# Kernel tuning notes

Measured on AMD Instinct MI355X. Metric: run time of the kernel, lower is better.

The kernel has to match this reference:

```python
import math
import jax, jax.numpy as jnp
from jax import lax
import numpy as np

NUM_POINTS = 256      # K sampled points
HIDDEN_DIM = 768
NUM_FREQS = 10
INPUT_DIM = 3 * 2 * NUM_FREQS  # 60


def _fps_indices(pts, k):
    """Furthest point sampling indices for a single cloud pts: [N,3] -> [k] int32.
    Standard iterative FPS starting from index 0."""
    n = pts.shape[0]
    idxs0 = jnp.zeros((k,), dtype=jnp.int32)
    dists0 = jnp.full((n,), jnp.inf, dtype=pts.dtype)

    def body(i, state):
        idxs, dists = state
        last = pts[idxs[i - 1]]                       # [3]
        d = jnp.sum((pts - last) ** 2, axis=-1)       # [N]
        dists = jnp.minimum(dists, d)
        idxs = idxs.at[i].set(jnp.argmax(dists).astype(jnp.int32))
        return (idxs, dists)

    idxs, _ = lax.fori_loop(1, k, body, (idxs0, dists0))
    return idxs


def setup_inputs() -> dict:
    key = jax.random.key(0)
    k1, k2, k3 = jax.random.split(key, 3)
    B, N = 32, 262144
    point_cloud = jax.random.normal(k1, (B, N, 3), dtype=jnp.float32)
    # Xavier-uniform Linear weight [out, in], zero bias (matches _init_weights)
    limit = math.sqrt(6.0 / (INPUT_DIM + HIDDEN_DIM))
    W = jax.random.uniform(k2, (HIDDEN_DIM, INPUT_DIM), jnp.float32, -limit, limit)
    b = jnp.zeros((HIDDEN_DIM,), dtype=jnp.float32)
    return {"point_cloud": point_cloud, "W": W, "b": b}


def reference(point_cloud, W, b):
    B = point_cloud.shape[0]
    # sanitize non-finite (matches torch.where(isfinite, x, 0))
    pc = jnp.where(jnp.isfinite(point_cloud), point_cloud, 0.0)

    # --- furthest point sampling (indices are non-differentiable) ---
    idxs = jax.vmap(lambda p: _fps_indices(lax.stop_gradient(p), NUM_POINTS))(pc)  # [B,K]
    sampled = jnp.take_along_axis(pc, idxs[:, :, None], axis=1)  # [B,K,3]

    # --- per-sample normalization: center then scale by max bbox dim ---
    centroid = jnp.mean(sampled, axis=1, keepdims=True)           # [B,1,3]
    centered = sampled - centroid                                  # [B,K,3]
    bbox = jnp.max(centered, axis=1) - jnp.min(centered, axis=1)   # [B,3]
    max_dim = jnp.max(bbox, axis=-1)                               # [B]
    scale = jnp.where(max_dim > 1e-8, max_dim, 1.0)
    normed = centered / scale[:, None, None]                       # [B,K,3]

    # --- Fourier encoding: sin/cos of coords * 2^f * pi ---
    freqs = jnp.power(2.0, jnp.arange(NUM_FREQS, dtype=jnp.float32))  # [F]
    scaled = normed[..., None] * freqs * jnp.float32(math.pi)         # [B,K,3,F]
    enc = jnp.stack([jnp.sin(scaled), jnp.cos(scaled)], axis=-1)      # [B,K,3,F,2]
    enc = enc.reshape(B, NUM_POINTS, INPUT_DIM)                       # [B,K,60]

    # --- linear projection (torch Linear: x @ W.T + b) ---
    return jnp.einsum('bkd,hd->bkh', enc, W) + b                      # [B,K,768]
```

## Files before the change

### kernel.cpp

```cpp
#include <hip/hip_runtime.h>

#define BATCH 32
#define NPTS  262144
#define KSAMP 256
#define NF    10
#define INDIM 60
#define HID   768

#define NBLK_PER_B 8
#define SLICE (NPTS/NBLK_PER_B)
#define REG_G 4
#define LDS_G 3

#define PI_F 3.14159274101257324f
#define PAY56 0x00FFFFFFFFFFFFFFull

typedef float v2f __attribute__((ext_vector_type(2)));

__device__ float g_px[BATCH*NPTS];
__device__ float g_py[BATCH*NPTS];
__device__ float g_pz[BATCH*NPTS];
__device__ float g_samp[BATCH*KSAMP*3];
__device__ float g_enc[(size_t)BATCH*KSAMP*INDIM];
__device__ float g_Wt[INDIM*HID];
__device__ unsigned long long g_slot[BATCH][2][NBLK_PER_B];

__device__ __forceinline__ float san(float v){
  float m = v*0.0f;
  return (m == 0.0f) ? v : 0.0f;
}

__device__ __forceinline__ unsigned long long shfl64_xor(unsigned long long v, int m){
  unsigned lo = __shfl_xor((unsigned)v, m);
  unsigned hi = __shfl_xor((unsigned)(v>>32), m);
  return ((unsigned long long)hi<<32)|lo;
}
__device__ __forceinline__ unsigned long long shfl64(unsigned long long v, int src){
  unsigned lo = __shfl((unsigned)v, src);
  unsigned hi = __shfl((unsigned)(v>>32), src);
  return ((unsigned long long)hi<<32)|lo;
}

__global__ __launch_bounds__(256) void region_prepass(const float* __restrict__ pc){
  int bid = blockIdx.x;
  int b   = bid >> 5;
  int rem = bid & 31;
  int q   = rem*1024 + threadIdx.x*4;
  int s   = q >> 12;
  int o   = q & 4095;
  int p   = s*SLICE + 7*4096 + o;
  const float* src = pc + ((size_t)b*NPTS + p)*3;
  float4 A = *(const float4*)(src);
  float4 Bv= *(const float4*)(src+4);
  float4 C = *(const float4*)(src+8);
  float v[12] = {A.x,A.y,A.z,A.w,Bv.x,Bv.y,Bv.z,Bv.w,C.x,C.y,C.z,C.w};
#pragma unroll
  for (int j=0;j<12;j++) v[j] = san(v[j]);
  size_t base = (size_t)b*NPTS + p;
  *(float4*)(g_px+base) = make_float4(v[0],v[3],v[6],v[9]);
  *(float4*)(g_py+base) = make_float4(v[1],v[4],v[7],v[10]);
  *(float4*)(g_pz+base) = make_float4(v[2],v[5],v[8],v[11]);
}

__global__ __launch_bounds__(256) void wtrans(const float* __restrict__ W){
  int idx = blockIdx.x*256 + threadIdx.x;
  int d = idx / HID;
  int h = idx - d*HID;
  g_Wt[idx] = W[h*INDIM + d];
  if (blockIdx.x == 0 && threadIdx.x < 256){
    ((unsigned long long*)g_slot)[threadIdx.x*2+0] = 0ull;
    ((unsigned long long*)g_slot)[threadIdx.x*2+1] = 0ull;
  }
}

__global__ __attribute__((amdgpu_flat_work_group_size(1024,1024)))
           __attribute__((amdgpu_waves_per_eu(4,4)))
void fps_kernel(const float* __restrict__ pc){
#pragma clang fp contract(off)
  __shared__ float4 sX[LDS_G*1024], sY[LDS_G*1024], sZ[LDS_G*1024];
  __shared__ unsigned long long s_cand[16];
  __shared__ float s_res[4];

  const int blk = blockIdx.x;
  const int b   = (blk & 7) + 8*(blk >> 6);
  const int s   = (blk >> 3) & 7;
  const int tid = threadIdx.x;
  const int lane = tid & 63, wave = tid >> 6;
  const size_t bN = (size_t)b*NPTS;
  const int soff = s*SLICE;

  v2f rx2[REG_G*2], ry2[REG_G*2], rz2[REG_G*2];
#pragma unroll
  for (int j=0;j<REG_G+LDS_G;j++){
    int p0 = soff + j*4096 + tid*4;
    const float* src = pc + (bN + p0)*3;
    float4 A = *(const float4*)(src);
    float4 Bv= *(const float4*)(src+4);
    float4 C = *(const float4*)(src+8);
    float v[12] = {A.x,A.y,A.z,A.w,Bv.x,Bv.y,Bv.z,Bv.w,C.x,C.y,C.z,C.w};
#pragma unroll
    for (int q=0;q<12;q++) v[q] = san(v[q]);
    if (j < REG_G){
      rx2[j*2+0] = (v2f){v[0], v[3]};  rx2[j*2+1] = (v2f){v[6], v[9]};
      ry2[j*2+0] = (v2f){v[1], v[4]};  ry2[j*2+1] = (v2f){v[7], v[10]};
      rz2[j*2+0] = (v2f){v[2], v[5]};  rz2[j*2+1] = (v2f){v[8], v[11]};
    } else {
      sX[(j-REG_G)*1024+tid] = make_float4(v[0],v[3],v[6],v[9]);
      sY[(j-REG_G)*1024+tid] = make_float4(v[1],v[4],v[7],v[10]);
      sZ[(j-REG_G)*1024+tid] = make_float4(v[2],v[5],v[8],v[11]);
    }
  }

  float d[32];
#pragma unroll
  for (int i=0;i<32;i++) d[i] = __builtin_huge_valf();

  float lx = san(pc[bN*3+0]), ly = san(pc[bN*3+1]), lz = san(pc[bN*3+2]);
  if (s==0 && tid<3) g_samp[(size_t)b*KSAMP*3 + tid] = san(pc[bN*3 + tid]);
  __syncthreads();

  const size_t gb = bN + soff + (size_t)7*4096 + tid*4;

  for (int k=1; k<KSAMP; k++){
    const int par = k & 1;
    const unsigned long long tagk = (unsigned long long)(unsigned)k << 56;
    float4 gx = *(const float4*)(g_px+gb);
    float4 gy = *(const float4*)(g_py+gb);
    float4 gz = *(const float4*)(g_pz+gb);

    v2f l2x = (v2f){lx,lx}, l2y = (v2f){ly,ly}, l2z = (v2f){lz,lz};

    float bestv = -1.0f; int bestc = 0;

#define UPD2(X2,Y2,Z2, DI) { \
      v2f dx_ = (X2) - l2x, dy_ = (Y2) - l2y, dz_ = (Z2) - l2z; \
      v2f dd_ = ((dx_*dx_) + (dy_*dy_)) + (dz_*dz_); \
      float nd0_ = fminf(d[DI], dd_.x);  d[DI] = nd0_; \
      if (nd0_ > bestv){ bestv = nd0_; bestc = (DI); } \
      float nd1_ = fminf(d[(DI)+1], dd_.y);  d[(DI)+1] = nd1_; \
      if (nd1_ > bestv){ bestv = nd1_; bestc = (DI)+1; } }

#pragma unroll
    for (int p=0;p<REG_G*2;p++)
      UPD2(rx2[p], ry2[p], rz2[p], p*2)
#pragma unroll
    for (int j=0;j<LDS_G;j++){
      float4 X = sX[j*1024+tid], Y = sY[j*1024+tid], Z = sZ[j*1024+tid];
      v2f Xa=(v2f){X.x,X.y}, Xb=(v2f){X.z,X.w};
      v2f Ya=(v2f){Y.x,Y.y}, Yb=(v2f){Y.z,Y.w};
      v2f Za=(v2f){Z.x,Z.y}, Zb=(v2f){Z.z,Z.w};
      UPD2(Xa, Ya, Za, (REG_G+j)*4)
      UPD2(Xb, Yb, Zb, (REG_G+j)*4+2)
    }
    {
      v2f Xa=(v2f){gx.x,gx.y}, Xb=(v2f){gx.z,gx.w};
      v2f Ya=(v2f){gy.x,gy.y}, Yb=(v2f){gy.z,gy.w};
      v2f Za=(v2f){gz.x,gz.y}, Zb=(v2f){gz.z,gz.w};
      UPD2(Xa, Ya, Za, 28)
      UPD2(Xb, Yb, Zb, 30)
    }
#undef UPD2

    int besti = soff + ((bestc>>2)<<12) + (tid<<2) + (bestc&3);

#pragma unroll
    for (int off=32; off; off>>=1){
      float ov = __shfl_down(bestv, off);
      int   oi = __shfl_down(besti, off);
      if (ov > bestv || (ov == bestv && oi < besti)){ bestv=ov; besti=oi; }
    }
    if (lane==0)
      s_cand[wave] = ((unsigned long long)__float_as_uint(bestv) << 24)
                   | (unsigned long long)(0xFFFFFFu ^ (unsigned)besti);

    __syncthreads();

    if (wave==0){
      unsigned long long pay = (lane < 16) ? s_cand[lane] : 0ull;
#pragma unroll
      for (int m=1; m<16; m<<=1){
        unsigned long long o = shfl64_xor(pay, m);
        if (o > pay) pay = o;
      }
      if (lane==0)
        __hip_atomic_store(&g_slot[b][par][s], tagk | pay,
                           __ATOMIC_RELAXED, __HIP_MEMORY_SCOPE_AGENT);
      unsigned long long gpay = 0;
      if (lane < NBLK_PER_B){
        unsigned long long gv;
        for (;;){
          gv = __hip_atomic_load(&g_slot[b][par][lane],
                                 __ATOMIC_RELAXED, __HIP_MEMORY_SCOPE_AGENT);
          if ((unsigned)(gv >> 56) == (unsigned)k) break;
        }
        gpay = gv & PAY56;
      }
#pragma unroll
      for (int m=1; m<8; m<<=1){
        unsigned long long o = shfl64_xor(gpay, m);
        if (o > gpay) gpay = o;
      }
      unsigned long long wing = shfl64(gpay, 0);
      unsigned w = 0xFFFFFFu ^ (unsigned)(wing & 0xFFFFFFu);
      int wu = __builtin_amdgcn_readfirstlane((int)w);
      if (lane < 3){
        float cv = san(pc[(bN + (size_t)(unsigned)wu)*3 + lane]);
        s_res[lane] = cv;
        if (s==0) g_samp[((size_t)b*KSAMP + k)*3 + lane] = cv;
      }
    }

    __syncthreads();
    lx = s_res[0]; ly = s_res[1]; lz = s_res[2];
  }
}

template<int OP>
__device__ __forceinline__ float blk_red(float v, float* s4){
  int tid = threadIdx.x;
#pragma unroll
  for (int off=32; off; off>>=1){
    float o = __shfl_down(v, off);
    v = (OP==0) ? v+o : ((OP==1) ? fmaxf(v,o) : fminf(v,o));
  }
  if ((tid&63)==0) s4[tid>>6] = v;
  __syncthreads();
  float r0=s4[0], r1=s4[1], r2=s4[2], r3=s4[3];
  float r = (OP==0) ? ((r0+r1)+(r2+r3))
          : ((OP==1) ? fmaxf(fmaxf(r0,r1),fmaxf(r2,r3))
                     : fminf(fminf(r0,r1),fminf(r2,r3)));
  __syncthreads();
  return r;
}

__global__ __launch_bounds__(256) void norm_encode(){
  __shared__ float s4[4];
  int b = blockIdx.x, k = threadIdx.x;
  const float* sp = &g_samp[((size_t)b*KSAMP + k)*3];
  float x = sp[0], y = sp[1], z = sp[2];

  float cx = blk_red<0>(x, s4) * (1.0f/KSAMP);
  float cy = blk_red<0>(y, s4) * (1.0f/KSAMP);
  float cz = blk_red<0>(z, s4) * (1.0f/KSAMP);

  float ux = __fsub_rn(x,cx), uy = __fsub_rn(y,cy), uz = __fsub_rn(z,cz);

  float mxx = blk_red<1>(ux, s4), mnx = blk_red<2>(ux, s4);
  float mxy = blk_red<1>(uy, s4), mny = blk_red<2>(uy, s4);
  float mxz = blk_red<1>(uz, s4), mnz = blk_red<2>(uz, s4);
  float bx = __fsub_rn(mxx,mnx), by = __fsub_rn(mxy,mny), bz = __fsub_rn(mxz,mnz);
  float md = fmaxf(fmaxf(bx,by),bz);
  float scale = (md > 1e-8f) ? md : 1.0f;

  float n3[3] = { __fdiv_rn(ux,scale), __fdiv_rn(uy,scale), __fdiv_rn(uz,scale) };

  float* e = &g_enc[((size_t)b*KSAMP + k)*INDIM];
#pragma unroll
  for (int c=0;c<3;c++){
    float base = n3[c];
#pragma unroll
    for (int f=0; f<NF; f++){
      float t = __fmul_rn(base, (float)(1<<f));
      float a = __fmul_rn(t, PI_F);
      e[c*2*NF + f*2 + 0] = sinf(a);
      e[c*2*NF + f*2 + 1] = cosf(a);
    }
  }
}

__global__ __launch_bounds__(256) void gemm_kernel(const float* __restrict__ bias,
                                                   float* __restrict__ out){
  __shared__ float s_enc[4*INDIM];
  int blk = blockIdx.x, tid = threadIdx.x;
  int row0 = blk*4;
  if (tid < 4*INDIM) s_enc[tid] = g_enc[(size_t)row0*INDIM + tid];
  __syncthreads();

  float acc[4][3] = {};
  for (int d=0; d<INDIM; d++){
    float w0 = g_Wt[d*HID + tid];
    float w1 = g_Wt[d*HID + tid + 256];
    float w2 = g_Wt[d*HID + tid + 512];
#pragma unroll
    for (int r=0;r<4;r++){
      float ev = s_enc[r*INDIM + d];
      acc[r][0] = fmaf(ev, w0, acc[r][0]);
      acc[r][1] = fmaf(ev, w1, acc[r][1]);
      acc[r][2] = fmaf(ev, w2, acc[r][2]);
    }
  }
  float b0=bias[tid], b1=bias[tid+256], b2=bias[tid+512];
#pragma unroll
  for (int r=0;r<4;r++){
    size_t o = (size_t)(row0+r)*HID;
    out[o+tid]     = acc[r][0]+b0;
    out[o+tid+256] = acc[r][1]+b1;
    out[o+tid+512] = acc[r][2]+b2;
  }
}

extern "C" void kernel_launch(void* const* d_in, const int* in_sizes, int n_in,
                              void* d_out, int out_size, void* d_ws, size_t ws_size,
                              hipStream_t stream){
  const float* pc   = (const float*)d_in[0];
  const float* W    = (const float*)d_in[1];
  const float* bias = (const float*)d_in[2];
  float* out = (float*)d_out;

  region_prepass<<<1024, 256, 0, stream>>>(pc);
  wtrans        <<<(INDIM*HID)/256, 256, 0, stream>>>(W);

  void* args[] = { (void*)&pc };
  hipLaunchCooperativeKernel((void*)fps_kernel, dim3(BATCH*NBLK_PER_B), dim3(1024),
                             args, 0, stream);

  norm_encode<<<BATCH, KSAMP, 0, stream>>>();
  gemm_kernel<<<(BATCH*KSAMP)/4, 256, 0, stream>>>(bias, out);
}
```

Baseline: 1.330 ms.

## Split FPS blocks into two independent half-block batches with flag-based sync

Each 1024-thread FPS block now serves two batches, one per 512-thread half, and every batch is spread over 16 slices instead of 8. The per-iteration __syncthreads barriers become LDS atomic tag slots and release/acquire flags, so the two halves advance independently and interleave their latency-bound reduction phases. It also adds s_sleep staggering and s_setprio around the critical path. The cost is a wider cross-block exchange (16 slots per batch) and spin-waiting, which may contend or be fragile with respect to LDS memory ordering.

```diff
diff --git a/kernel.cpp b/kernel.cpp
--- a/kernel.cpp
+++ b/kernel.cpp
@@ -7,8 +7,10 @@
 #define INDIM 60
 #define HID   768
 
-#define NBLK_PER_B 8
-#define SLICE (NPTS/NBLK_PER_B)
+#define NSLICE 16
+#define TPB_H  512
+#define SLICE  (NPTS/NSLICE)
+#define GPTS   (TPB_H*4)
 #define REG_G 4
 #define LDS_G 3
 
@@ -23,7 +25,7 @@
 __device__ float g_samp[BATCH*KSAMP*3];
 __device__ float g_enc[(size_t)BATCH*KSAMP*INDIM];
 __device__ float g_Wt[INDIM*HID];
-__device__ unsigned long long g_slot[BATCH][2][NBLK_PER_B];
+__device__ unsigned long long g_slot[BATCH][2][NSLICE];
 
 __device__ __forceinline__ float san(float v){
   float m = v*0.0f;
@@ -46,9 +48,9 @@
   int b   = bid >> 5;
   int rem = bid & 31;
   int q   = rem*1024 + threadIdx.x*4;
-  int s   = q >> 12;
-  int o   = q & 4095;
-  int p   = s*SLICE + 7*4096 + o;
+  int s   = q >> 11;
+  int o   = q & 2047;
+  int p   = s*SLICE + 7*GPTS + o;
   const float* src = pc + ((size_t)b*NPTS + p)*3;
   float4 A = *(const float4*)(src);
   float4 Bv= *(const float4*)(src+4);
@@ -67,9 +69,10 @@
   int d = idx / HID;
   int h = idx - d*HID;
   g_Wt[idx] = W[h*INDIM + d];
-  if (blockIdx.x == 0 && threadIdx.x < 256){
-    ((unsigned long long*)g_slot)[threadIdx.x*2+0] = 0ull;
-    ((unsigned long long*)g_slot)[threadIdx.x*2+1] = 0ull;
+  if (blockIdx.x == 0){
+#pragma unroll
+    for (int r=0;r<4;r++)
+      ((unsigned long long*)g_slot)[threadIdx.x + 256*r] = 0ull;
   }
 }
 
@@ -77,22 +80,28 @@
            __attribute__((amdgpu_waves_per_eu(4,4)))
 void fps_kernel(const float* __restrict__ pc){
 #pragma clang fp contract(off)
-  __shared__ float4 sX[LDS_G*1024], sY[LDS_G*1024], sZ[LDS_G*1024];
-  __shared__ unsigned long long s_cand[16];
-  __shared__ float s_res[4];
+  __shared__ float4 sX[2*LDS_G*TPB_H], sY[2*LDS_G*TPB_H], sZ[2*LDS_G*TPB_H];
+  __shared__ unsigned long long s_cand[2][2][8];
+  __shared__ float s_res[2][2][4];
+  __shared__ int   s_flag[2][2];
 
   const int blk = blockIdx.x;
-  const int b   = (blk & 7) + 8*(blk >> 6);
-  const int s   = (blk >> 3) & 7;
+  const int xcd = blk & 7;
+  const int jj  = blk >> 3;
   const int tid = threadIdx.x;
-  const int lane = tid & 63, wave = tid >> 6;
+  const int half  = tid >> 9;
+  const int tid_h = tid & 511;
+  const int lane  = tid & 63;
+  const int wv    = (tid >> 6) & 7;
+  const int s   = jj & 15;
+  const int b   = 4*xcd + (jj >> 4) + 2*half;
   const size_t bN = (size_t)b*NPTS;
   const int soff = s*SLICE;
 
   v2f rx2[REG_G*2], ry2[REG_G*2], rz2[REG_G*2];
 #pragma unroll
   for (int j=0;j<REG_G+LDS_G;j++){
-    int p0 = soff + j*4096 + tid*4;
+    int p0 = soff + j*GPTS + tid_h*4;
     const float* src = pc + (bN + p0)*3;
     float4 A = *(const float4*)(src);
     float4 Bv= *(const float4*)(src+4);
@@ -105,9 +114,10 @@
       ry2[j*2+0] = (v2f){v[1], v[4]};  ry2[j*2+1] = (v2f){v[7], v[10]};
       rz2[j*2+0] = (v2f){v[2], v[5]};  rz2[j*2+1] = (v2f){v[8], v[11]};
     } else {
-      sX[(j-REG_G)*1024+tid] = make_float4(v[0],v[3],v[6],v[9]);
-      sY[(j-REG_G)*1024+tid] = make_float4(v[1],v[4],v[7],v[10]);
-      sZ[(j-REG_G)*1024+tid] = make_float4(v[2],v[5],v[8],v[11]);
+      int li = (half*LDS_G + (j-REG_G))*TPB_H + tid_h;
+      sX[li] = make_float4(v[0],v[3],v[6],v[9]);
+      sY[li] = make_float4(v[1],v[4],v[7],v[10]);
+      sZ[li] = make_float4(v[2],v[5],v[8],v[11]);
     }
   }
 
@@ -116,10 +126,14 @@
   for (int i=0;i<32;i++) d[i] = __builtin_huge_valf();
 
   float lx = san(pc[bN*3+0]), ly = san(pc[bN*3+1]), lz = san(pc[bN*3+2]);
-  if (s==0 && tid<3) g_samp[(size_t)b*KSAMP*3 + tid] = san(pc[bN*3 + tid]);
+  if (s==0 && tid_h<3) g_samp[(size_t)b*KSAMP*3 + tid_h] = san(pc[bN*3 + tid_h]);
+  if (tid < 4)  ((int*)s_flag)[tid] = 0;
+  if (tid < 32) ((unsigned long long*)s_cand)[tid] = 0ull;
   __syncthreads();
 
-  const size_t gb = bN + soff + (size_t)7*4096 + tid*4;
+  if (half) __builtin_amdgcn_s_sleep(62);
+
+  const size_t gb = bN + soff + (size_t)7*GPTS + tid_h*4;
 
   for (int k=1; k<KSAMP; k++){
     const int par = k & 1;
@@ -145,7 +159,8 @@
       UPD2(rx2[p], ry2[p], rz2[p], p*2)
 #pragma unroll
     for (int j=0;j<LDS_G;j++){
-      float4 X = sX[j*1024+tid], Y = sY[j*1024+tid], Z = sZ[j*1024+tid];
+      int li = (half*LDS_G + j)*TPB_H + tid_h;
+      float4 X = sX[li], Y = sY[li], Z = sZ[li];
       v2f Xa=(v2f){X.x,X.y}, Xb=(v2f){X.z,X.w};
       v2f Ya=(v2f){Y.x,Y.y}, Yb=(v2f){Y.z,Y.w};
       v2f Za=(v2f){Z.x,Z.y}, Zb=(v2f){Z.z,Z.w};
@@ -161,7 +176,7 @@
     }
 #undef UPD2
 
-    int besti = soff + ((bestc>>2)<<12) + (tid<<2) + (bestc&3);
+    int besti = soff + ((bestc>>2)<<11) + (tid_h<<2) + (bestc&3);
 
 #pragma unroll
     for (int off=32; off; off>>=1){
@@ -169,34 +184,41 @@
       int   oi = __shfl_down(besti, off);
       if (ov > bestv || (ov == bestv && oi < besti)){ bestv=ov; besti=oi; }
     }
+    unsigned long long wkey = tagk
+                            | ((unsigned long long)__float_as_uint(bestv) << 24)
+                            | (unsigned long long)(0xFFFFFFu ^ (unsigned)besti);
     if (lane==0)
-      s_cand[wave] = ((unsigned long long)__float_as_uint(bestv) << 24)
-                   | (unsigned long long)(0xFFFFFFu ^ (unsigned)besti);
-
-    __syncthreads();
-
-    if (wave==0){
-      unsigned long long pay = (lane < 16) ? s_cand[lane] : 0ull;
-#pragma unroll
-      for (int m=1; m<16; m<<=1){
+      __hip_atomic_store(&s_cand[half][par][wv], wkey,
+                         __ATOMIC_RELAXED, __HIP_MEMORY_SCOPE_WORKGROUP);
+
+    if (wv==0){
+      unsigned long long pay;
+      for (;;){
+        pay = __hip_atomic_load(&s_cand[half][par][lane & 7],
+                                __ATOMIC_RELAXED, __HIP_MEMORY_SCOPE_WORKGROUP);
+        if ((unsigned)(pay >> 56) == (unsigned)k) break;
+        __builtin_amdgcn_s_sleep(1);
+      }
+      pay &= PAY56;
+#pragma unroll
+      for (int m=1; m<8; m<<=1){
         unsigned long long o = shfl64_xor(pay, m);
         if (o > pay) pay = o;
       }
       if (lane==0)
         __hip_atomic_store(&g_slot[b][par][s], tagk | pay,
                            __ATOMIC_RELAXED, __HIP_MEMORY_SCOPE_AGENT);
-      unsigned long long gpay = 0;
-      if (lane < NBLK_PER_B){
-        unsigned long long gv;
-        for (;;){
-          gv = __hip_atomic_load(&g_slot[b][par][lane],
+      unsigned long long gpay;
+      for (;;){
+        gpay = __hip_atomic_load(&g_slot[b][par][lane & 15],
                                  __ATOMIC_RELAXED, __HIP_MEMORY_SCOPE_AGENT);
-          if ((unsigned)(gv >> 56) == (unsigned)k) break;
-        }
-        gpay = gv & PAY56;
-      }
-#pragma unroll
-      for (int m=1; m<8; m<<=1){
+        if ((unsigned)(gpay >> 56) == (unsigned)k) break;
+        __builtin_amdgcn_s_sleep(2);
+      }
+      __builtin_amdgcn_s_setprio(1);
+      gpay &= PAY56;
+#pragma unroll
+      for (int m=1; m<16; m<<=1){
         unsigned long long o = shfl64_xor(gpay, m);
         if (o > gpay) gpay = o;
       }
@@ -205,13 +227,20 @@
       int wu = __builtin_amdgcn_readfirstlane((int)w);
       if (lane < 3){
         float cv = san(pc[(bN + (size_t)(unsigned)wu)*3 + lane]);
-        s_res[lane] = cv;
+        s_res[half][par][lane] = cv;
         if (s==0) g_samp[((size_t)b*KSAMP + k)*3 + lane] = cv;
       }
-    }
-
-    __syncthreads();
-    lx = s_res[0]; ly = s_res[1]; lz = s_res[2];
+      if (lane==0)
+        __hip_atomic_store(&s_flag[half][par], k,
+                           __ATOMIC_RELEASE, __HIP_MEMORY_SCOPE_WORKGROUP);
+      __builtin_amdgcn_s_setprio(0);
+      lx = s_res[half][par][0]; ly = s_res[half][par][1]; lz = s_res[half][par][2];
+    } else {
+      while (__hip_atomic_load(&s_flag[half][par],
+                               __ATOMIC_ACQUIRE, __HIP_MEMORY_SCOPE_WORKGROUP) != k)
+        __builtin_amdgcn_s_sleep(1);
+      lx = s_res[half][par][0]; ly = s_res[half][par][1]; lz = s_res[half][par][2];
+    }
   }
 }
 
@@ -311,7 +340,7 @@
   wtrans        <<<(INDIM*HID)/256, 256, 0, stream>>>(W);
 
   void* args[] = { (void*)&pc };
-  hipLaunchCooperativeKernel((void*)fps_kernel, dim3(BATCH*NBLK_PER_B), dim3(1024),
+  hipLaunchCooperativeKernel((void*)fps_kernel, dim3(BATCH*NSLICE/2), dim3(1024),
                              args, 0, stream);
 
   norm_encode<<<BATCH, KSAMP, 0, stream>>>();
```

Result: slower. 1.517 ms (+14.1%).
